# Optimization experiments

Hardware: AMD Instinct MI355X
Metric: run time of the kernel (lower is better)

Reference implementation:

```python
import jax, jax.numpy as jnp
import numpy as np

B, T, D, S = 32, 4096, 512, 256
SCALE = 0.1  # time_bias_scale


def setup_inputs() -> dict:
    key = jax.random.key(0)
    ks = jax.random.split(key, 9)
    return {
        "context": jax.random.normal(ks[0], (B, T, D), jnp.float32),
        "t_star": jax.random.uniform(ks[1], (B,), jnp.float32),
        "t_context": jax.random.uniform(ks[2], (B, T, 1), jnp.float32),
        "W1": jax.random.normal(ks[3], (1, D), jnp.float32) / np.sqrt(1.0),
        "b1": jax.random.normal(ks[4], (D,), jnp.float32) * 0.02,
        "W2": jax.random.normal(ks[5], (D, D), jnp.float32) / np.sqrt(D),
        "b2": jax.random.normal(ks[6], (D,), jnp.float32) * 0.02,
        "Wout": jax.random.normal(ks[7], (D, 2 * S), jnp.float32) / np.sqrt(D),
        "bout": jax.random.normal(ks[8], (2 * S,), jnp.float32) * 0.02,
    }


def reference(context, t_star, t_context, W1, b1, W2, b2, Wout, bout):
    # query embed: Linear(1,D) -> SiLU -> Linear(D,D)
    h = jax.nn.silu(t_star[:, None] @ W1 + b1)        # (B, D)
    q = h @ W2 + b2                                   # (B, D)
    # single-query attention scores with additive time bias
    scores = jnp.einsum('bd,btd->bt', q, context)     # (B, T)
    time_bias = -jnp.abs(t_star[:, None] - t_context[..., 0]) / SCALE  # (B, T)
    weights = jax.nn.softmax(scores + time_bias, axis=-1)
    pooled = jnp.einsum('bt,btd->bd', weights, context)  # (B, D)
    out = pooled @ Wout + bout                            # (B, 2S)
    mu, log_sigma = out[:, :S], out[:, S:]
    return (mu, log_sigma)
```

## Files before the change

kernel.cpp:

```cpp
#include <hip/hip_runtime.h>
#include <math.h>

#define BB 32
#define TT 4096
#define DD 512
#define SS 256
#define WPB 96
#define NBLK 768
static constexpr float INV_SCALE = 10.0f;

typedef float f32x4 __attribute__((ext_vector_type(4)));

__global__ __launch_bounds__(512) void k_q(
    const float* __restrict__ t_star, const float* __restrict__ W1,
    const float* __restrict__ b1, const float* __restrict__ W2,
    const float* __restrict__ b2, float* __restrict__ q,
    int* __restrict__ cnt) {
  const int b   = blockIdx.x >> 3;
  const int jg  = blockIdx.x & 7;
  const int tid = threadIdx.x;
  const int di  = tid & 63;
  const int kg  = tid >> 6;
  if (tid == 0 && blockIdx.x < BB) cnt[blockIdx.x] = 0;
  __shared__ float h[DD];
  __shared__ float red[8][64];
  {
    float x = t_star[b] * W1[tid] + b1[tid];
    h[tid] = x / (1.0f + __expf(-x));
  }
  __syncthreads();
  const float* w = W2 + jg * 64 + di;
  float acc = 0.0f;
#pragma unroll 8
  for (int kk = 0; kk < 64; ++kk) {
    const int k = kg * 64 + kk;
    acc += h[k] * w[(size_t)k * DD];
  }
  red[kg][di] = acc;
  __syncthreads();
  if (tid < 64) {
    float s = 0.0f;
#pragma unroll
    for (int g = 0; g < 8; ++g) s += red[g][tid];
    q[b * DD + jg * 64 + tid] = s + b2[jg * 64 + tid];
  }
}

#define GLDS(gp, lp)                                                        \
  __builtin_amdgcn_global_load_lds(                                         \
      (const __attribute__((address_space(1))) void*)(gp),                  \
      (__attribute__((address_space(3))) void*)(lp), 16, 0, 2 )

__global__ __launch_bounds__(256) void k_fused(
    const float* __restrict__ ctx, const float* __restrict__ q,
    const float* __restrict__ t_star, const float* __restrict__ t_ctx,
    float* __restrict__ part_pool,
    float* __restrict__ part_ms) {
  __shared__ __align__(16) float lds[4][3][2 * DD];
  const int wid  = threadIdx.x >> 6;
  const int lane = threadIdx.x & 63;
  const int W    = blockIdx.x * 4 + wid;
  const int b    = W / WPB;
  const int v    = W % WPB;
  const int NG   = (v < 32) ? 22 : 21;

  const float4* qp = (const float4*)(q + b * DD);
  const float4 q0 = qp[lane];
  const float4 q1 = qp[64 + lane];
  const float ts = t_star[b];

  const int lg = lane & 31;
  int gidx = lg * WPB + v;
  if (gidx >= TT / 2) gidx = v;
  const float2 tc = *(const float2*)(t_ctx + b * TT + 2 * gidx);
  const float tbx = -fabsf(ts - tc.x) * INV_SCALE;
  const float tby = -fabsf(ts - tc.y) * INV_SCALE;

  float m = -INFINITY, l = 0.0f;
  float4 p0 = {0, 0, 0, 0}, p1 = {0, 0, 0, 0};

  const float* cbatch = ctx + (size_t)b * TT * DD;

#pragma unroll
  for (int g = 0; g < 2; ++g) {
    const float* gb = cbatch + (size_t)(g * WPB + v) * 2 * DD;
    float* sb = &lds[wid][g][0];
#pragma unroll
    for (int piece = 0; piece < 4; ++piece)
      GLDS(gb + piece * 256 + lane * 4, sb + piece * 256);
  }

  int rs = 0, wslot = 2;
  for (int g = 0; g < NG; ++g) {
    if (g + 2 < NG) {
      const float* gb = cbatch + (size_t)((g + 2) * WPB + v) * 2 * DD;
      float* sb = &lds[wid][wslot][0];
#pragma unroll
      for (int piece = 0; piece < 4; ++piece)
        GLDS(gb + piece * 256 + lane * 4, sb + piece * 256);
      asm volatile("s_waitcnt vmcnt(8)" ::: "memory");
    } else if (g + 2 == NG) {
      asm volatile("s_waitcnt vmcnt(4)" ::: "memory");
    } else {
      asm volatile("s_waitcnt vmcnt(0)" ::: "memory");
    }

    const float4* sf = (const float4*)&lds[wid][rs][0];
    const float4 x0 = sf[lane];
    const float4 x1 = sf[64 + lane];
    const float4 y0 = sf[128 + lane];
    const float4 y1 = sf[192 + lane];

    float s0 = x0.x * q0.x + x0.y * q0.y + x0.z * q0.z + x0.w * q0.w +
               x1.x * q1.x + x1.y * q1.y + x1.z * q1.z + x1.w * q1.w;
    float s1 = y0.x * q0.x + y0.y * q0.y + y0.z * q0.z + y0.w * q0.w +
               y1.x * q1.x + y1.y * q1.y + y1.z * q1.z + y1.w * q1.w;
#pragma unroll
    for (int off = 32; off > 0; off >>= 1) {
      s0 += __shfl_xor(s0, off);
      s1 += __shfl_xor(s1, off);
    }
    s0 += __shfl(tbx, g);
    s1 += __shfl(tby, g);

    const float gm = fmaxf(s0, s1);
    const float nm = fmaxf(m, gm);
    const float sc = __expf(m - nm);
    m = nm;
    const float e0 = __expf(s0 - m);
    const float e1 = __expf(s1 - m);
    l = l * sc + e0 + e1;
    p0.x = p0.x * sc + e0 * x0.x + e1 * y0.x;
    p0.y = p0.y * sc + e0 * x0.y + e1 * y0.y;
    p0.z = p0.z * sc + e0 * x0.z + e1 * y0.z;
    p0.w = p0.w * sc + e0 * x0.w + e1 * y0.w;
    p1.x = p1.x * sc + e0 * x1.x + e1 * y1.x;
    p1.y = p1.y * sc + e0 * x1.y + e1 * y1.y;
    p1.z = p1.z * sc + e0 * x1.z + e1 * y1.z;
    p1.w = p1.w * sc + e0 * x1.w + e1 * y1.w;

    rs = (rs == 2) ? 0 : rs + 1;
    wslot = (wslot == 2) ? 0 : wslot + 1;
  }

  f32x4* pp = (f32x4*)(part_pool + (size_t)W * DD);
  f32x4 v0 = {p0.x, p0.y, p0.z, p0.w};
  f32x4 v1 = {p1.x, p1.y, p1.z, p1.w};
  __builtin_nontemporal_store(v0, pp + lane);
  __builtin_nontemporal_store(v1, pp + 64 + lane);
  if (lane == 0) {
    part_ms[W * 2 + 0] = m;
    part_ms[W * 2 + 1] = l;
  }
}

__global__ __launch_bounds__(512) void k_merge_out(
    const float* __restrict__ part_pool, const float* __restrict__ part_ms,
    const float* __restrict__ Wout, const float* __restrict__ bout,
    float* __restrict__ pool, int* __restrict__ cnt, float* __restrict__ out) {
  const int b   = blockIdx.x >> 3;
  const int dg  = blockIdx.x & 7;
  const int tid = threadIdx.x;
  const int lane = tid & 63;
  const int base = b * WPB;
  __shared__ float scl[WPB];
  __shared__ float red[8][64];
  __shared__ float pool_s[DD];

  const float mA = part_ms[(base + lane) * 2 + 0];
  const float lA = part_ms[(base + lane) * 2 + 1];
  float mB = -INFINITY, lB = 0.0f;
  if (lane < WPB - 64) {
    mB = part_ms[(base + 64 + lane) * 2 + 0];
    lB = part_ms[(base + 64 + lane) * 2 + 1];
  }
  float M = fmaxf(mA, mB);
#pragma unroll
  for (int off = 32; off > 0; off >>= 1) M = fmaxf(M, __shfl_xor(M, off));
  float Z = __expf(mA - M) * lA + ((lane < WPB - 64) ? __expf(mB - M) * lB : 0.0f);
#pragma unroll
  for (int off = 32; off > 0; off >>= 1) Z += __shfl_xor(Z, off);
  const float invZ = 1.0f / Z;
  if (tid < WPB) scl[tid] = __expf(part_ms[(base + tid) * 2] - M);
  __syncthreads();

  const int dl = tid & 63;
  const int cg = tid >> 6;
  const int d  = dg * 64 + dl;
  float acc = 0.0f;
#pragma unroll
  for (int i = 0; i < 12; ++i) {
    const int c = cg * 12 + i;
    acc += scl[c] *
           __builtin_nontemporal_load(&part_pool[((size_t)base + c) * DD + d]);
  }
  red[cg][dl] = acc;
  __syncthreads();
  if (tid < 64) {
    float s = 0.0f;
#pragma unroll
    for (int g = 0; g < 8; ++g) s += red[g][tid];
    pool[b * DD + dg * 64 + tid] = s * invZ;
  }
  __syncthreads();

  if (tid == 0) {
    __threadfence();
    atomicAdd(&cnt[b], 1);
    while (atomicAdd(&cnt[b], 0) < 8) __builtin_amdgcn_s_sleep(8);
    __threadfence();
  }
  __syncthreads();

  pool_s[tid] = pool[b * DD + tid];
  if (tid < DD - 512) {}
  __syncthreads();

  const int j  = dg * 64 + (tid & 63);
  const int kg = tid >> 6;
  float a2 = 0.0f;
#pragma unroll 8
  for (int kk = 0; kk < 64; ++kk) {
    const int k = kg * 64 + kk;
    a2 += pool_s[k] * Wout[(size_t)k * DD + j];
  }
  red[kg][tid & 63] = a2;
  __syncthreads();
  if (tid < 64) {
    const int jj = dg * 64 + tid;
    float o = bout[jj];
#pragma unroll
    for (int g = 0; g < 8; ++g) o += red[g][tid];
    if (jj < SS) out[b * SS + jj] = o;
    else         out[BB * SS + b * SS + (jj - SS)] = o;
  }
}

extern "C" void kernel_launch(void* const* d_in, const int* in_sizes, int n_in,
                              void* d_out, int out_size, void* d_ws, size_t ws_size,
                              hipStream_t stream) {
  const float* ctx    = (const float*)d_in[0];
  const float* t_star = (const float*)d_in[1];
  const float* t_ctx  = (const float*)d_in[2];
  const float* W1     = (const float*)d_in[3];
  const float* b1     = (const float*)d_in[4];
  const float* W2     = (const float*)d_in[5];
  const float* b2     = (const float*)d_in[6];
  const float* Wout   = (const float*)d_in[7];
  const float* bout   = (const float*)d_in[8];
  float* out = (float*)d_out;

  float* ws = (float*)d_ws;
  float* q         = ws;
  float* part_pool = q + (size_t)BB * DD;
  float* part_ms   = part_pool + (size_t)BB * WPB * DD;
  float* pool      = part_ms + (size_t)BB * WPB * 2;
  int*   cnt       = (int*)(pool + (size_t)BB * DD);

  k_q<<<BB * 8, 512, 0, stream>>>(t_star, W1, b1, W2, b2, q, cnt);
  k_fused<<<NBLK, 256, 0, stream>>>(ctx, q, t_star, t_ctx, part_pool, part_ms);
  k_merge_out<<<BB * 8, 512, 0, stream>>>(part_pool, part_ms, Wout, bout,
                                          pool, cnt, out);
}
```

Baseline: 72.33 us.

## Replace inter-block counter sync with redundant per-block merge of partials

The epilogue no longer splits the partial-pool merge across 8 blocks per batch and then spin-waits on a global atomic counter. Each of the 8 blocks now merges all 96 partials for the full 512-wide vector itself, then does its slice of the output projection. This removes the counter reset, the atomic spin and the global pool round trip, at the cost of 8x redundant partial-pool reads, mostly served from L2. Nontemporal stores and loads of the partials become ordinary ones, so they can stay cached for those repeated reads.

Measured after the change: 66.87 us. 1.08x faster.

```diff
diff --git a/kernel.cpp b/kernel.cpp
--- a/kernel.cpp
+++ b/kernel.cpp
@@ -9,19 +9,15 @@
 #define NBLK 768
 static constexpr float INV_SCALE = 10.0f;
 
-typedef float f32x4 __attribute__((ext_vector_type(4)));
-
 __global__ __launch_bounds__(512) void k_q(
     const float* __restrict__ t_star, const float* __restrict__ W1,
     const float* __restrict__ b1, const float* __restrict__ W2,
-    const float* __restrict__ b2, float* __restrict__ q,
-    int* __restrict__ cnt) {
+    const float* __restrict__ b2, float* __restrict__ q) {
   const int b   = blockIdx.x >> 3;
   const int jg  = blockIdx.x & 7;
   const int tid = threadIdx.x;
   const int di  = tid & 63;
   const int kg  = tid >> 6;
-  if (tid == 0 && blockIdx.x < BB) cnt[blockIdx.x] = 0;
   __shared__ float h[DD];
   __shared__ float red[8][64];
   {
@@ -143,29 +139,27 @@
     wslot = (wslot == 2) ? 0 : wslot + 1;
   }
 
-  f32x4* pp = (f32x4*)(part_pool + (size_t)W * DD);
-  f32x4 v0 = {p0.x, p0.y, p0.z, p0.w};
-  f32x4 v1 = {p1.x, p1.y, p1.z, p1.w};
-  __builtin_nontemporal_store(v0, pp + lane);
-  __builtin_nontemporal_store(v1, pp + 64 + lane);
+  float4* pp = (float4*)(part_pool + (size_t)W * DD);
+  pp[lane] = p0;
+  pp[64 + lane] = p1;
   if (lane == 0) {
     part_ms[W * 2 + 0] = m;
     part_ms[W * 2 + 1] = l;
   }
 }
 
-__global__ __launch_bounds__(512) void k_merge_out(
+__global__ __launch_bounds__(512) void k_epi(
     const float* __restrict__ part_pool, const float* __restrict__ part_ms,
     const float* __restrict__ Wout, const float* __restrict__ bout,
-    float* __restrict__ pool, int* __restrict__ cnt, float* __restrict__ out) {
+    float* __restrict__ out) {
   const int b   = blockIdx.x >> 3;
-  const int dg  = blockIdx.x & 7;
+  const int jg  = blockIdx.x & 7;
   const int tid = threadIdx.x;
   const int lane = tid & 63;
   const int base = b * WPB;
   __shared__ float scl[WPB];
+  __shared__ float pool_s[DD];
   __shared__ float red[8][64];
-  __shared__ float pool_s[DD];
 
   const float mA = part_ms[(base + lane) * 2 + 0];
   const float lA = part_ms[(base + lane) * 2 + 1];
@@ -184,39 +178,16 @@
   if (tid < WPB) scl[tid] = __expf(part_ms[(base + tid) * 2] - M);
   __syncthreads();
 
-  const int dl = tid & 63;
-  const int cg = tid >> 6;
-  const int d  = dg * 64 + dl;
-  float acc = 0.0f;
-#pragma unroll
-  for (int i = 0; i < 12; ++i) {
-    const int c = cg * 12 + i;
-    acc += scl[c] *
-           __builtin_nontemporal_load(&part_pool[((size_t)base + c) * DD + d]);
-  }
-  red[cg][dl] = acc;
-  __syncthreads();
-  if (tid < 64) {
-    float s = 0.0f;
-#pragma unroll
-    for (int g = 0; g < 8; ++g) s += red[g][tid];
-    pool[b * DD + dg * 64 + tid] = s * invZ;
-  }
-  __syncthreads();
-
-  if (tid == 0) {
-    __threadfence();
-    atomicAdd(&cnt[b], 1);
-    while (atomicAdd(&cnt[b], 0) < 8) __builtin_amdgcn_s_sleep(8);
-    __threadfence();
-  }
-  __syncthreads();
-
-  pool_s[tid] = pool[b * DD + tid];
-  if (tid < DD - 512) {}
-  __syncthreads();
-
-  const int j  = dg * 64 + (tid & 63);
+  {
+    float acc = 0.0f;
+#pragma unroll 8
+    for (int c = 0; c < WPB; ++c)
+      acc += scl[c] * part_pool[((size_t)base + c) * DD + tid];
+    pool_s[tid] = acc * invZ;
+  }
+  __syncthreads();
+
+  const int j  = jg * 64 + (tid & 63);
   const int kg = tid >> 6;
   float a2 = 0.0f;
 #pragma unroll 8
@@ -227,7 +198,7 @@
   red[kg][tid & 63] = a2;
   __syncthreads();
   if (tid < 64) {
-    const int jj = dg * 64 + tid;
+    const int jj = jg * 64 + tid;
     float o = bout[jj];
 #pragma unroll
     for (int g = 0; g < 8; ++g) o += red[g][tid];
@@ -254,11 +225,8 @@
   float* q         = ws;
   float* part_pool = q + (size_t)BB * DD;
   float* part_ms   = part_pool + (size_t)BB * WPB * DD;
-  float* pool      = part_ms + (size_t)BB * WPB * 2;
-  int*   cnt       = (int*)(pool + (size_t)BB * DD);
-
-  k_q<<<BB * 8, 512, 0, stream>>>(t_star, W1, b1, W2, b2, q, cnt);
+
+  k_q<<<BB * 8, 512, 0, stream>>>(t_star, W1, b1, W2, b2, q);
   k_fused<<<NBLK, 256, 0, stream>>>(ctx, q, t_star, t_ctx, part_pool, part_ms);
-  k_merge_out<<<BB * 8, 512, 0, stream>>>(part_pool, part_ms, Wout, bout,
-                                          pool, cnt, out);
-}
+  k_epi<<<BB * 8, 512, 0, stream>>>(part_pool, part_ms, Wout, bout, out);
+}
```
